# Kernel optimization log

Hardware: AMD Instinct MI355X
Metric: run time of the kernel (lower is better)

The kernel has to match this reference:

```python
import jax, jax.numpy as jnp
import numpy as np

G = 512  # canvas resolution (init arg)

def setup_inputs() -> dict:
    key = jax.random.key(0)
    k1, k2 = jax.random.split(key)
    strokes = jax.random.uniform(k1, (32, 8, 2), dtype=jnp.float32)   # [S,P,2] in [0,1]
    thicknesses = jax.random.uniform(k2, (32,), dtype=jnp.float32)    # [S]
    return {"strokes": strokes, "thicknesses": thicknesses}

def reference(strokes, thicknesses):
    # strokes: [S,P,2], thicknesses: [S]. Vectorized version of the per-stroke loop.
    g = jnp.float32(G)
    s = jnp.clip(strokes, 0.0, 1.0) * g                      # [S,P,2] pixel coords
    t = jnp.maximum(thicknesses * 2.0 + 0.5, 0.5)            # [S] stroke thickness
    v = s[:, :-1][:, :, None, None, :]                       # [S,P-1,1,1,2] segment starts
    w = s[:, 1:][:, :, None, None, :]                        # [S,P-1,1,1,2] segment ends
    idx = jnp.arange(G, dtype=jnp.float32)
    xs, ys = jnp.meshgrid(idx, idx, indexing='ij')
    p = jnp.stack((xs, ys), axis=-1)[None, None]             # [1,1,G,G,2] grid coords
    e = w - v                                                # segment direction
    d2 = jnp.sum(e * e, axis=-1)                             # [S,P-1,1,1] squared length
    pv = p - v                                               # [S,P-1,G,G,2]
    frac = jnp.clip(jnp.sum(pv * e, axis=-1) / (d2 + 1e-5), 0.0, 1.0)  # [S,P-1,G,G]
    dist = jnp.linalg.norm(pv - frac[..., None] * e, axis=-1)  # point-to-segment distance
    darkness = jnp.min(dist, axis=1) / (2.0 * t[:, None, None])  # [S,G,G] min over segments
    return jnp.minimum(jnp.min(darkness, axis=0), 1.0)          # min over strokes vs ones-grid
```

## Files before the change

kernel.cpp:

```cpp
#include <hip/hip_runtime.h>


#define NSEG 224

__global__ __launch_bounds__(256) void render_kernel(
    const float* __restrict__ strokes,
    const float* __restrict__ thick,
    float* __restrict__ out)
{
    __shared__ float4 sseg[NSEG];
    __shared__ float2 smul[NSEG];
    const int tid = threadIdx.x;

    if (tid < NSEG) {
        const int s = tid / 7;
        const int k = tid - s * 7;
        const int base = (s * 8 + k) * 2;
        float ax = strokes[base + 0];
        float ay = strokes[base + 1];
        float bx = strokes[base + 2];
        float by = strokes[base + 3];
        ax = fminf(fmaxf(ax, 0.0f), 1.0f) * 512.0f;
        ay = fminf(fmaxf(ay, 0.0f), 1.0f) * 512.0f;
        bx = fminf(fmaxf(bx, 0.0f), 1.0f) * 512.0f;
        by = fminf(fmaxf(by, 0.0f), 1.0f) * 512.0f;
        const float ex = bx - ax;
        const float ey = by - ay;
        const float d2 = ex * ex + ey * ey;
        const float t  = fmaxf(thick[s] * 2.0f + 0.5f, 0.5f);
        sseg[tid] = make_float4(ax, ay, ex, ey);
        smul[tid] = make_float2(1.0f / (d2 + 1e-5f), 1.0f / (4.0f * t * t));
    }
    __syncthreads();

    const int n   = (blockIdx.x * 256 + tid) * 2;
    const float px  = (float)(n >> 9);
    const float py0 = (float)(n & 511);
    const float py1 = py0 + 1.0f;

    float acc0 = 1e30f, acc1 = 1e30f;
#pragma unroll 4
    for (int g = 0; g < NSEG; ++g) {
        const float4 sg = sseg[g];
        const float2 ms = smul[g];
        const float pvx  = px  - sg.x;
        const float pvy0 = py0 - sg.y;
        const float pvy1 = py1 - sg.y;
        const float pe   = pvx * sg.z;
        float f0 = fmaf(pvy0, sg.w, pe) * ms.x;
        float f1 = fmaf(pvy1, sg.w, pe) * ms.x;
        f0 = fminf(fmaxf(f0, 0.0f), 1.0f);
        f1 = fminf(fmaxf(f1, 0.0f), 1.0f);
        const float dx0 = fmaf(-f0, sg.z, pvx);
        const float dy0 = fmaf(-f0, sg.w, pvy0);
        const float dx1 = fmaf(-f1, sg.z, pvx);
        const float dy1 = fmaf(-f1, sg.w, pvy1);
        const float q0 = fmaf(dy0, dy0, dx0 * dx0);
        const float q1 = fmaf(dy1, dy1, dx1 * dx1);
        acc0 = fminf(acc0, q0 * ms.y);
        acc1 = fminf(acc1, q1 * ms.y);
    }

    const float o0 = fminf(sqrtf(acc0), 1.0f);
    const float o1 = fminf(sqrtf(acc1), 1.0f);
    *reinterpret_cast<float2*>(out + n) = make_float2(o0, o1);
}

extern "C" void kernel_launch(void* const* d_in, const int* in_sizes, int n_in,
                              void* d_out, int out_size, void* d_ws, size_t ws_size,
                              hipStream_t stream) {
    const float* strokes = (const float*)d_in[0];
    const float* thick   = (const float*)d_in[1];
    float* out = (float*)d_out;
    hipLaunchKernelGGL(render_kernel, dim3(512), dim3(256), 0, stream,
                       strokes, thick, out);
}
```

Before: 67.49 us.

## Cull segments per 2D tile using distance bound before per-pixel loop

Each block now covers a 16x32 pixel tile instead of a row strip. Each segment is tested against the tile centre with a bound of 2t plus the tile half-diagonal, and only segments that can affect the tile are compacted into shared memory through an atomic counter. The per-pixel loop then runs only over the kept segments and starts its accumulator at 4, so anything beyond the clamp is ignored. This removes most of the distance evaluations but adds an atomic and a loop with a runtime trip count that is no longer unrolled, and blocks can end up with uneven amounts of work.

```diff
diff --git a/kernel.cpp b/kernel.cpp
--- a/kernel.cpp
+++ b/kernel.cpp
@@ -2,6 +2,8 @@
 
 
 #define NSEG 224
+#define TILE_I 16
+#define TILE_J 32
 
 __global__ __launch_bounds__(256) void render_kernel(
     const float* __restrict__ strokes,
@@ -10,7 +12,18 @@
 {
     __shared__ float4 sseg[NSEG];
     __shared__ float2 smul[NSEG];
+    __shared__ int cnt;
     const int tid = threadIdx.x;
+
+    const int tile_j = blockIdx.x & 15;
+    const int tile_i = blockIdx.x >> 4;
+    const int i0 = tile_i * TILE_I;
+    const int j0 = tile_j * TILE_J;
+    const float ccx = (float)i0 + 7.5f;
+    const float ccy = (float)j0 + 15.5f;
+
+    if (tid == 0) cnt = 0;
+    __syncthreads();
 
     if (tid < NSEG) {
         const int s = tid / 7;
@@ -27,20 +40,33 @@
         const float ex = bx - ax;
         const float ey = by - ay;
         const float d2 = ex * ex + ey * ey;
+        const float inv = 1.0f / (d2 + 1e-5f);
         const float t  = fmaxf(thick[s] * 2.0f + 0.5f, 0.5f);
-        sseg[tid] = make_float4(ax, ay, ex, ey);
-        smul[tid] = make_float2(1.0f / (d2 + 1e-5f), 1.0f / (4.0f * t * t));
+        const float pvx = ccx - ax;
+        const float pvy = ccy - ay;
+        float f = fmaf(pvy, ey, pvx * ex) * inv;
+        f = fminf(fmaxf(f, 0.0f), 1.0f);
+        const float dx = fmaf(-f, ex, pvx);
+        const float dy = fmaf(-f, ey, pvy);
+        const float d2c = fmaf(dy, dy, dx * dx);
+        const float thr = 2.0f * t + 18.0f;
+        if (d2c < thr * thr) {
+            const int idx = atomicAdd(&cnt, 1);
+            sseg[idx] = make_float4(ax, ay, ex, ey);
+            smul[idx] = make_float2(inv, 1.0f / (4.0f * t * t));
+        }
     }
     __syncthreads();
+    const int n_kept = cnt;
 
-    const int n   = (blockIdx.x * 256 + tid) * 2;
-    const float px  = (float)(n >> 9);
-    const float py0 = (float)(n & 511);
+    const int pi = i0 + (tid >> 4);
+    const int pj = j0 + ((tid & 15) << 1);
+    const float px  = (float)pi;
+    const float py0 = (float)pj;
     const float py1 = py0 + 1.0f;
 
-    float acc0 = 1e30f, acc1 = 1e30f;
-#pragma unroll 4
-    for (int g = 0; g < NSEG; ++g) {
+    float acc0 = 4.0f, acc1 = 4.0f;
+    for (int g = 0; g < n_kept; ++g) {
         const float4 sg = sseg[g];
         const float2 ms = smul[g];
         const float pvx  = px  - sg.x;
@@ -63,7 +89,7 @@
 
     const float o0 = fminf(sqrtf(acc0), 1.0f);
     const float o1 = fminf(sqrtf(acc1), 1.0f);
-    *reinterpret_cast<float2*>(out + n) = make_float2(o0, o1);
+    *reinterpret_cast<float2*>(out + (pi << 9) + pj) = make_float2(o0, o1);
 }
 
 extern "C" void kernel_launch(void* const* d_in, const int* in_sizes, int n_in,
```

Measured after the change: 55.93 us. 17.1% less time.
